# Kernel tuning notes

Measured on AMD Instinct MI355X. Metric: run time of the kernel, lower is better.

Reference implementation:

```python
import jax, jax.numpy as jnp
import numpy as np

N_EMBD = 1024
N_HEAD = 16
HEAD_DIM = N_EMBD // N_HEAD
B, T = 2, 2048
EPS = 1e-5


def setup_inputs() -> dict:
    key = jax.random.key(0)
    ks = jax.random.split(key, 12)
    s = lambda fan_in: 1.0 / np.sqrt(fan_in)
    return {
        "x": jax.random.normal(ks[0], (B, T, N_EMBD), dtype=jnp.float32),
        "ln1_g": jnp.ones((N_EMBD,), jnp.float32),
        "ln1_b": jnp.zeros((N_EMBD,), jnp.float32),
        "W_attn": jax.random.normal(ks[1], (N_EMBD, 3 * N_EMBD), jnp.float32) * s(N_EMBD),
        "b_attn": jnp.zeros((3 * N_EMBD,), jnp.float32),
        "W_proj": jax.random.normal(ks[2], (N_EMBD, N_EMBD), jnp.float32) * s(N_EMBD),
        "b_proj": jnp.zeros((N_EMBD,), jnp.float32),
        "ln2_g": jnp.ones((N_EMBD,), jnp.float32),
        "ln2_b": jnp.zeros((N_EMBD,), jnp.float32),
        "W_fc": jax.random.normal(ks[3], (N_EMBD, 4 * N_EMBD), jnp.float32) * s(N_EMBD),
        "b_fc": jnp.zeros((4 * N_EMBD,), jnp.float32),
        "W_fc2": jax.random.normal(ks[4], (4 * N_EMBD, N_EMBD), jnp.float32) * s(4 * N_EMBD),
        "b_fc2": jnp.zeros((N_EMBD,), jnp.float32),
    }


def _layernorm(x, g, b):
    mu = jnp.mean(x, axis=-1, keepdims=True)
    var = jnp.mean(jnp.square(x - mu), axis=-1, keepdims=True)
    return (x - mu) * jax.lax.rsqrt(var + EPS) * g + b


def _attention(x, W_attn, b_attn, W_proj, b_proj):
    Bsz, Tlen, C = x.shape
    qkv = x @ W_attn + b_attn  # [B,T,3C]
    q, k, v = jnp.split(qkv, 3, axis=-1)
    # [B,H,T,D]
    q = q.reshape(Bsz, Tlen, N_HEAD, HEAD_DIM).transpose(0, 2, 1, 3)
    k = k.reshape(Bsz, Tlen, N_HEAD, HEAD_DIM).transpose(0, 2, 1, 3)
    v = v.reshape(Bsz, Tlen, N_HEAD, HEAD_DIM).transpose(0, 2, 1, 3)
    att = jnp.einsum("bhqd,bhkd->bhqk", q, k) * (HEAD_DIM ** -0.5)
    causal = jnp.tril(jnp.ones((Tlen, Tlen), dtype=bool))
    att = jnp.where(causal[None, None], att, -jnp.inf)
    att = jax.nn.softmax(att, axis=-1)
    y = jnp.einsum("bhqk,bhkd->bhqd", att, v)
    y = y.transpose(0, 2, 1, 3).reshape(Bsz, Tlen, C)
    return y @ W_proj + b_proj


def _mlp(x, W_fc, b_fc, W_fc2, b_fc2):
    h = jax.nn.gelu(x @ W_fc + b_fc, approximate=False)
    return h @ W_fc2 + b_fc2


def reference(x, ln1_g, ln1_b, W_attn, b_attn, W_proj, b_proj,
              ln2_g, ln2_b, W_fc, b_fc, W_fc2, b_fc2):
    x = x + _attention(_layernorm(x, ln1_g, ln1_b), W_attn, b_attn, W_proj, b_proj)
    x = x + _mlp(_layernorm(x, ln2_g, ln2_b), W_fc, b_fc, W_fc2, b_fc2)
    return x
```

## Files before the change

### kernel.cpp

```cpp
#include <hip/hip_runtime.h>
#include <math.h>

typedef unsigned short ushort_t;
typedef __attribute__((ext_vector_type(8))) short f16x8;
typedef __attribute__((ext_vector_type(4))) float f32x4;

#define N_EMBD 1024
#define N_HEAD 16
#define HEAD_DIM 64
#define SEQ_B 2
#define SEQ_T 2048
#define M_TOK (SEQ_B * SEQ_T)

__device__ __forceinline__ ushort_t f2b(float f) {
    union { float f; unsigned int u; } v; v.f = f;
    unsigned int r = (v.u + 0x7FFFu + ((v.u >> 16) & 1u)) >> 16;
    return (ushort_t)r;
}

__device__ __forceinline__ float gelu_fast(float v) {
    float u = v + 0.044715f * v * v * v;
    float e = __expf(-1.5957691216057308f * u);
    return v * __frcp_rn(1.0f + e);
}

__device__ __forceinline__ void gload_lds16(const ushort_t* g, ushort_t* l) {
    __builtin_amdgcn_global_load_lds(
        (const __attribute__((address_space(1))) void*)g,
        (__attribute__((address_space(3))) void*)l, 16, 0, 0);
}

__global__ __launch_bounds__(256) void prep_w(
    const float* __restrict__ Wa, const float* __restrict__ Wp,
    const float* __restrict__ Wf, const float* __restrict__ Wf2,
    ushort_t* __restrict__ Ta, ushort_t* __restrict__ Tp,
    ushort_t* __restrict__ Tf, ushort_t* __restrict__ Tf2,
    const float* __restrict__ x, const float* __restrict__ g1,
    const float* __restrict__ b1, ushort_t* __restrict__ xn) {
    int b = blockIdx.x;
    int t = threadIdx.x;
    if (b >= 12288) {
        int row = b - 12288;
        const float4 v = ((const float4*)(x + (size_t)row * N_EMBD))[t];
        float s = v.x + v.y + v.z + v.w;
        float s2 = v.x * v.x + v.y * v.y + v.z * v.z + v.w * v.w;
        for (int m = 1; m < 64; m <<= 1) {
            s += __shfl_xor(s, m, 64);
            s2 += __shfl_xor(s2, m, 64);
        }
        __shared__ float ss[4], ss2[4];
        if ((t & 63) == 0) { ss[t >> 6] = s; ss2[t >> 6] = s2; }
        __syncthreads();
        s = ss[0] + ss[1] + ss[2] + ss[3];
        s2 = ss2[0] + ss2[1] + ss2[2] + ss2[3];
        float mu = s * (1.0f / N_EMBD);
        float var = s2 * (1.0f / N_EMBD) - mu * mu;
        float rs = rsqrtf(var + 1e-5f);
        const float4 gg = ((const float4*)g1)[t];
        const float4 bb = ((const float4*)b1)[t];
        ushort_t o4[4];
        o4[0] = f2b((v.x - mu) * rs * gg.x + bb.x);
        o4[1] = f2b((v.y - mu) * rs * gg.y + bb.y);
        o4[2] = f2b((v.z - mu) * rs * gg.z + bb.z);
        o4[3] = f2b((v.w - mu) * rs * gg.w + bb.w);
        *(ushort4*)(xn + (size_t)row * N_EMBD + t * 4) = *(ushort4*)o4;
        return;
    }
    __shared__ float tile[32][33];
    const float* W; ushort_t* T; int K, N, nx;
    if (b < 3072)      { W = Wa;  T = Ta;  K = 1024; N = 3072; nx = 96; }
    else if (b < 4096) { W = Wp;  T = Tp;  K = 1024; N = 1024; nx = 32; b -= 3072; }
    else if (b < 8192) { W = Wf;  T = Tf;  K = 1024; N = 4096; nx = 128; b -= 4096; }
    else               { W = Wf2; T = Tf2; K = 4096; N = 1024; nx = 32; b -= 8192; }
    int n0 = (b % nx) * 32, k0 = (b / nx) * 32;
    for (int i = 0; i < 4; ++i) {
        int l = t + i * 256; int r = l >> 5, c2 = l & 31;
        tile[r][c2] = W[(size_t)(k0 + r) * N + n0 + c2];
    }
    __syncthreads();
    for (int i = 0; i < 4; ++i) {
        int l = t + i * 256; int r = l >> 5, c2 = l & 31;
        T[(size_t)(n0 + r) * K + k0 + c2] = f2b(tile[c2][r]);
    }
}

__global__ __launch_bounds__(256) void ln2_kernel(
    const float* __restrict__ x, const float* __restrict__ g,
    const float* __restrict__ b, ushort_t* __restrict__ out) {
    int row = blockIdx.x;
    int t = threadIdx.x;
    const float4 v = ((const float4*)(x + (size_t)row * N_EMBD))[t];
    float s = v.x + v.y + v.z + v.w;
    float s2 = v.x * v.x + v.y * v.y + v.z * v.z + v.w * v.w;
    for (int m = 1; m < 64; m <<= 1) {
        s += __shfl_xor(s, m, 64);
        s2 += __shfl_xor(s2, m, 64);
    }
    __shared__ float ss[4], ss2[4];
    if ((t & 63) == 0) { ss[t >> 6] = s; ss2[t >> 6] = s2; }
    __syncthreads();
    s = ss[0] + ss[1] + ss[2] + ss[3];
    s2 = ss2[0] + ss2[1] + ss2[2] + ss2[3];
    float mu = s * (1.0f / N_EMBD);
    float var = s2 * (1.0f / N_EMBD) - mu * mu;
    float rs = rsqrtf(var + 1e-5f);
    const float4 gg = ((const float4*)g)[t];
    const float4 bb = ((const float4*)b)[t];
    ushort_t o4[4];
    o4[0] = f2b((v.x - mu) * rs * gg.x + bb.x);
    o4[1] = f2b((v.y - mu) * rs * gg.y + bb.y);
    o4[2] = f2b((v.z - mu) * rs * gg.z + bb.z);
    o4[3] = f2b((v.w - mu) * rs * gg.w + bb.w);
    *(ushort4*)(out + (size_t)row * N_EMBD + t * 4) = *(ushort4*)o4;
}

template <int MODE, int NJ>
__device__ __forceinline__ void gemm_epilogue(
    f32x4 (&acc)[4][NJ], const float* __restrict__ bias,
    const float* __restrict__ resid, void* __restrict__ Cout,
    int m0, int n0, int wr, int wc, int quad, int l16, int N) {
    for (int i = 0; i < 4; ++i) {
        for (int j = 0; j < NJ; ++j) {
            int col = n0 + wc + j * 16 + l16;
            float bv = bias[col];
            for (int r = 0; r < 4; ++r) {
                int row = m0 + wr + i * 16 + quad * 4 + r;
                float v = acc[i][j][r] + bv;
                if (MODE == 2) v = gelu_fast(v);
                if (MODE == 1 || MODE == 3) v += resid[(size_t)row * N + col];
                if (MODE == 0 || MODE == 2)
                    ((ushort_t*)Cout)[(size_t)row * N + col] = f2b(v);
                else
                    ((float*)Cout)[(size_t)row * N + col] = v;
            }
        }
    }
}

template <int MODE>
__device__ __forceinline__ void gemm_body_dma(
    const ushort_t* __restrict__ A, const ushort_t* __restrict__ Bt,
    const float* __restrict__ bias, const float* __restrict__ resid,
    void* __restrict__ Cout, int M, int N, int K) {
    __shared__ ushort_t As[2][128 * 32];
    __shared__ ushort_t Bs[2][128 * 32];
    int t = threadIdx.x;
    int wave = t >> 6, lane = t & 63;
    int quad = lane >> 4, l16 = lane & 15;
    const int swl = (l16 ^ (l16 >> 2)) & 3;
    int wr = (wave >> 1) * 64, wc = (wave & 1) * 64;
    const int m0 = blockIdx.y * 128, n0 = blockIdx.x * 128;

    const int c = wave * 64 + lane;
    const int srow = c >> 2, s_l = c & 3;
    const int s_g = s_l ^ ((srow ^ (srow >> 2)) & 3);
    const ushort_t* Ap = &A[(size_t)(m0 + srow) * K + s_g * 8];
    const ushort_t* Bp = &Bt[(size_t)(n0 + srow) * K + s_g * 8];

    const int NK = K >> 5;
    gload_lds16(Ap, &As[0][wave * 512]);
    gload_lds16(Ap + (size_t)64 * K, &As[0][wave * 512 + 2048]);
    gload_lds16(Bp, &Bs[0][wave * 512]);
    gload_lds16(Bp + (size_t)64 * K, &Bs[0][wave * 512 + 2048]);

    f32x4 acc[4][4] = {};
    for (int kt = 0; kt < NK; ++kt) {
        const int cur = kt & 1;
        __syncthreads();
        if (kt + 1 < NK) {
            const int nxt = cur ^ 1;
            const int k0 = (kt + 1) << 5;
            gload_lds16(Ap + k0, &As[nxt][wave * 512]);
            gload_lds16(Ap + (size_t)64 * K + k0, &As[nxt][wave * 512 + 2048]);
            gload_lds16(Bp + k0, &Bs[nxt][wave * 512]);
            gload_lds16(Bp + (size_t)64 * K + k0, &Bs[nxt][wave * 512 + 2048]);
        }
        f16x8 af[4], bf[4];
        for (int i = 0; i < 4; ++i)
            af[i] = *(const f16x8*)&As[cur][(wr + i * 16 + l16) * 32 + (quad ^ swl) * 8];
        for (int j = 0; j < 4; ++j)
            bf[j] = *(const f16x8*)&Bs[cur][(wc + j * 16 + l16) * 32 + (quad ^ swl) * 8];
        for (int i = 0; i < 4; ++i)
            for (int j = 0; j < 4; ++j)
                acc[i][j] = __builtin_amdgcn_mfma_f32_16x16x32_bf16(
                    af[i], bf[j], acc[i][j], 0, 0, 0);
    }
    gemm_epilogue<MODE, 4>(acc, bias, resid, Cout, m0, n0, wr, wc, quad, l16, N);
}

template <int MODE>
__device__ __forceinline__ void gemm_body_dma64(
    const ushort_t* __restrict__ A, const ushort_t* __restrict__ Bt,
    const float* __restrict__ bias, const float* __restrict__ resid,
    void* __restrict__ Cout, int M, int N, int K) {
    __shared__ ushort_t As[2][128 * 32];
    __shared__ ushort_t Bs[2][64 * 32];
    int t = threadIdx.x;
    int wave = t >> 6, lane = t & 63;
    int quad = lane >> 4, l16 = lane & 15;
    const int swl = (l16 ^ (l16 >> 2)) & 3;
    int wr = (wave >> 1) * 64, wc = (wave & 1) * 32;
    const int m0 = blockIdx.y * 128, n0 = blockIdx.x * 64;

    const int c = wave * 64 + lane;
    const int srow = c >> 2, s_l = c & 3;
    const int s_g = s_l ^ ((srow ^ (srow >> 2)) & 3);
    const ushort_t* Ap = &A[(size_t)(m0 + srow) * K + s_g * 8];
    const ushort_t* Bp = &Bt[(size_t)(n0 + srow) * K + s_g * 8];

    const int NK = K >> 5;
    gload_lds16(Ap, &As[0][wave * 512]);
    gload_lds16(Ap + (size_t)64 * K, &As[0][wave * 512 + 2048]);
    gload_lds16(Bp, &Bs[0][wave * 512]);

    f32x4 acc[4][2] = {};
    for (int kt = 0; kt < NK; ++kt) {
        const int cur = kt & 1;
        __syncthreads();
        if (kt + 1 < NK) {
            const int nxt = cur ^ 1;
            const int k0 = (kt + 1) << 5;
            gload_lds16(Ap + k0, &As[nxt][wave * 512]);
            gload_lds16(Ap + (size_t)64 * K + k0, &As[nxt][wave * 512 + 2048]);
            gload_lds16(Bp + k0, &Bs[nxt][wave * 512]);
        }
        f16x8 af[4], bf[2];
        for (int i = 0; i < 4; ++i)
            af[i] = *(const f16x8*)&As[cur][(wr + i * 16 + l16) * 32 + (quad ^ swl) * 8];
        for (int j = 0; j < 2; ++j)
            bf[j] = *(const f16x8*)&Bs[cur][(wc + j * 16 + l16) * 32 + (quad ^ swl) * 8];
        for (int i = 0; i < 4; ++i)
            for (int j = 0; j < 2; ++j)
                acc[i][j] = __builtin_amdgcn_mfma_f32_16x16x32_bf16(
                    af[i], bf[j], acc[i][j], 0, 0, 0);
    }
    gemm_epilogue<MODE, 2>(acc, bias, resid, Cout, m0, n0, wr, wc, quad, l16, N);
}

__global__ __launch_bounds__(256) void gemm_qkv(
    const ushort_t* A, const ushort_t* Bt, const float* bias, void* C,
    int M, int N, int K) { gemm_body_dma<0>(A, Bt, bias, nullptr, C, M, N, K); }
__global__ __launch_bounds__(256) void gemm_mlp1(
    const ushort_t* A, const ushort_t* Bt, const float* bias, void* C,
    int M, int N, int K) { gemm_body_dma<2>(A, Bt, bias, nullptr, C, M, N, K); }
__global__ __launch_bounds__(256) void gemm_proj(
    const ushort_t* A, const ushort_t* Bt, const float* bias,
    const float* resid, void* C, int M, int N, int K) {
    gemm_body_dma64<1>(A, Bt, bias, resid, C, M, N, K); }
__global__ __launch_bounds__(256) void gemm_out(
    const ushort_t* A, const ushort_t* Bt, const float* bias,
    const float* resid, void* C, int M, int N, int K) {
    gemm_body_dma64<3>(A, Bt, bias, resid, C, M, N, K); }

__global__ __launch_bounds__(256) void attn_kernel(
    const ushort_t* __restrict__ qkv, ushort_t* __restrict__ y) {
    const int bh = blockIdx.y;
    const int b = bh >> 4, h = bh & 15;
    const int tok0 = b * SEQ_T;
    const int t = threadIdx.x, wave = t >> 6, lane = t & 63;
    const int quad = lane >> 4, l16 = lane & 15;
    const int sw8 = l16 & 7;
    const size_t ld = 3 * N_EMBD;
    const ushort_t* Qb = qkv + (size_t)tok0 * ld + h * HEAD_DIM;
    const ushort_t* Kb = Qb + N_EMBD;
    const ushort_t* Vb = Qb + 2 * N_EMBD;

    __shared__ ushort_t Ks[64 * 64];
    __shared__ ushort_t Vt[64 * 64];
    __shared__ ushort_t Pl[4][16 * 64];

    const int kc = wave * 64 + lane;
    const int kv_s = kc >> 3, ks_l = kc & 7;
    const int ks_g = ks_l ^ (kv_s & 7);
    const ushort_t* KpL = Kb + (size_t)kv_s * ld + ks_g * 8;

    f16x8 onesB;
    for (int i = 0; i < 8; ++i) onesB[i] = (short)0x3F80;

    for (int phase = 0; phase < 2; ++phase) {
        const int qt = phase == 0 ? (int)blockIdx.x : 31 - (int)blockIdx.x;
        const int q0 = qt * 64;

        const int qrow = q0 + wave * 16 + l16;
        f16x8 qf0 = *(const f16x8*)&Qb[(size_t)qrow * ld + quad * 8];
        f16x8 qf1 = *(const f16x8*)&Qb[(size_t)qrow * ld + 32 + quad * 8];

        f32x4 o[4] = {};
        f32x4 lsum = {};

        const int nkt = qt + 1;
        for (int kt = 0; kt < nkt; ++kt) {
            __syncthreads();
            const ushort_t* kp = KpL + (size_t)kt * 64 * ld;
            gload_lds16(kp, &Ks[wave * 512]);
            gload_lds16(kp + (size_t)32 * ld, &Ks[wave * 512 + 2048]);
            for (int i = 0; i < 2; ++i) {
                int l = t + i * 256;
                int kv = l >> 3, dc = (l & 7) * 8;
                uint4 raw = *(const uint4*)&Vb[(size_t)(kt * 64 + kv) * ld + dc];
                const ushort_t* pv = (const ushort_t*)&raw;
                int pos = kv ^ ((l & 7) << 3);
                for (int e = 0; e < 8; ++e)
                    Vt[(dc + e) * 64 + pos] = pv[e];
            }
            __syncthreads();
            f32x4 s[4];
            const int ksl = (quad ^ sw8) * 8;
            for (int j = 0; j < 4; ++j) {
                const int kr = j * 16 + l16;
                f16x8 kf0 = *(const f16x8*)&Ks[kr * 64 + ksl];
                f16x8 kf1 = *(const f16x8*)&Ks[kr * 64 + (ksl ^ 32)];
                f32x4 z = {};
                z = __builtin_amdgcn_mfma_f32_16x16x32_bf16(qf0, kf0, z, 0, 0, 0);
                z = __builtin_amdgcn_mfma_f32_16x16x32_bf16(qf1, kf1, z, 0, 0, 0);
                s[j] = z;
            }
            if (kt == qt) {
                const int qr = wave * 16 + quad * 4;
                for (int j = 0; j < 4; ++j) {
                    int kg = j * 16 + l16;
                    for (int r = 0; r < 4; ++r)
                        if (kg > qr + r) s[j][r] = -INFINITY;
                }
            }
            ushort_t* myP = Pl[wave];
            for (int j = 0; j < 4; ++j) {
                int kvv = j * 16 + l16;
                int slotb = ((kvv >> 3) * 8);
                int klo = kvv & 7;
                for (int r = 0; r < 4; ++r) {
                    float p = __expf(__builtin_fmaf(s[j][r], 0.125f, -20.0f));
                    int q = quad * 4 + r;
                    myP[q * 64 + (slotb ^ ((q & 7) * 8)) + klo] = f2b(p);
                }
            }
            const int psl = (quad ^ sw8) * 8;
            f16x8 pa0 = *(const f16x8*)&myP[l16 * 64 + psl];
            f16x8 pa1 = *(const f16x8*)&myP[l16 * 64 + (psl ^ 32)];
            lsum = __builtin_amdgcn_mfma_f32_16x16x32_bf16(pa0, onesB, lsum, 0, 0, 0);
            lsum = __builtin_amdgcn_mfma_f32_16x16x32_bf16(pa1, onesB, lsum, 0, 0, 0);
            for (int dj = 0; dj < 4; ++dj) {
                const int d = dj * 16 + l16;
                const int dsw = ((d >> 3) & 7) * 8;
                f16x8 vb0 = *(const f16x8*)&Vt[d * 64 + ((quad * 8) ^ dsw)];
                f16x8 vb1 = *(const f16x8*)&Vt[d * 64 + (((quad * 8) ^ dsw) ^ 32)];
                f32x4 oo = o[dj];
                oo = __builtin_amdgcn_mfma_f32_16x16x32_bf16(pa0, vb0, oo, 0, 0, 0);
                oo = __builtin_amdgcn_mfma_f32_16x16x32_bf16(pa1, vb1, oo, 0, 0, 0);
                o[dj] = oo;
            }
        }
        float rl[4];
        for (int r = 0; r < 4; ++r) rl[r] = __frcp_rn(lsum[r]);
        for (int dj = 0; dj < 4; ++dj)
            for (int r = 0; r < 4; ++r) {
                int row = tok0 + q0 + wave * 16 + quad * 4 + r;
                int col = h * HEAD_DIM + dj * 16 + l16;
                y[(size_t)row * N_EMBD + col] = f2b(o[dj][r] * rl[r]);
            }
    }
}

extern "C" void kernel_launch(void* const* d_in, const int* in_sizes, int n_in,
                              void* d_out, int out_size, void* d_ws, size_t ws_size,
                              hipStream_t stream) {
    const float* x      = (const float*)d_in[0];
    const float* ln1_g  = (const float*)d_in[1];
    const float* ln1_b  = (const float*)d_in[2];
    const float* W_attn = (const float*)d_in[3];
    const float* b_attn = (const float*)d_in[4];
    const float* W_proj = (const float*)d_in[5];
    const float* b_proj = (const float*)d_in[6];
    const float* ln2_g  = (const float*)d_in[7];
    const float* ln2_b  = (const float*)d_in[8];
    const float* W_fc   = (const float*)d_in[9];
    const float* b_fc   = (const float*)d_in[10];
    const float* W_fc2  = (const float*)d_in[11];
    const float* b_fc2  = (const float*)d_in[12];
    float* out = (float*)d_out;

    char* w = (char*)d_ws;
    size_t o = 0;
    ushort_t* xn      = (ushort_t*)(w + o); o += (size_t)M_TOK * N_EMBD * 2;
    ushort_t* qkv     = (ushort_t*)(w + o); o += (size_t)M_TOK * 3 * N_EMBD * 2;
    ushort_t* y       = (ushort_t*)(w + o); o += (size_t)M_TOK * N_EMBD * 2;
    float*    x1      = (float*)(w + o);    o += (size_t)M_TOK * N_EMBD * 4;
    ushort_t* x1n     = (ushort_t*)(w + o); o += (size_t)M_TOK * N_EMBD * 2;
    ushort_t* hbuf    = (ushort_t*)(w + o); o += (size_t)M_TOK * 4 * N_EMBD * 2;
    ushort_t* Wt_attn = (ushort_t*)(w + o); o += (size_t)N_EMBD * 3 * N_EMBD * 2;
    ushort_t* Wt_proj = (ushort_t*)(w + o); o += (size_t)N_EMBD * N_EMBD * 2;
    ushort_t* Wt_fc   = (ushort_t*)(w + o); o += (size_t)N_EMBD * 4 * N_EMBD * 2;
    ushort_t* Wt_fc2  = (ushort_t*)(w + o); o += (size_t)4 * N_EMBD * N_EMBD * 2;

    prep_w<<<12288 + M_TOK, 256, 0, stream>>>(
        W_attn, W_proj, W_fc, W_fc2, Wt_attn, Wt_proj, Wt_fc, Wt_fc2,
        x, ln1_g, ln1_b, xn);
    gemm_qkv<<<dim3(3 * N_EMBD / 128, M_TOK / 128), 256, 0, stream>>>(
        xn, Wt_attn, b_attn, qkv, M_TOK, 3 * N_EMBD, N_EMBD);
    attn_kernel<<<dim3(SEQ_T / 128, SEQ_B * N_HEAD), 256, 0, stream>>>(qkv, y);
    gemm_proj<<<dim3(N_EMBD / 64, M_TOK / 128), 256, 0, stream>>>(
        y, Wt_proj, b_proj, x, x1, M_TOK, N_EMBD, N_EMBD);
    ln2_kernel<<<M_TOK, 256, 0, stream>>>(x1, ln2_g, ln2_b, x1n);
    gemm_mlp1<<<dim3(4 * N_EMBD / 128, M_TOK / 128), 256, 0, stream>>>(
        x1n, Wt_fc, b_fc, hbuf, M_TOK, 4 * N_EMBD, N_EMBD);
    gemm_out<<<dim3(N_EMBD / 64, M_TOK / 128), 256, 0, stream>>>(
        hbuf, Wt_fc2, b_fc2, x1, out, M_TOK, N_EMBD, 4 * N_EMBD);
    (void)in_sizes; (void)n_in; (void)out_size; (void)ws_size;
}
```

Baseline: 373.0 us.

## Split K across two wave groups inside proj and fc2 GEMM blocks

The proj and fc2 GEMMs now launch 512 threads per block. Each group of 4 waves processes half of the K dimension with its own double-buffered LDS tiles, and the partial sums are combined through LDS before the epilogue. The goal is more waves per tile and a shorter per-wave K loop, which adds latency hiding for these narrow-N GEMMs. In exchange the block uses twice the LDS and pays an extra reduction and sync, which may lower the number of blocks resident per CU.

```diff
diff --git a/kernel.cpp b/kernel.cpp
--- a/kernel.cpp
+++ b/kernel.cpp
@@ -189,29 +189,31 @@
 }
 
 template <int MODE>
-__device__ __forceinline__ void gemm_body_dma64(
+__device__ __forceinline__ void gemm_body_splitk(
     const ushort_t* __restrict__ A, const ushort_t* __restrict__ Bt,
     const float* __restrict__ bias, const float* __restrict__ resid,
     void* __restrict__ Cout, int M, int N, int K) {
-    __shared__ ushort_t As[2][128 * 32];
-    __shared__ ushort_t Bs[2][64 * 32];
+    __shared__ ushort_t As[2][2][128 * 32];
+    __shared__ ushort_t Bs[2][2][64 * 32];
     int t = threadIdx.x;
     int wave = t >> 6, lane = t & 63;
+    int half = wave >> 2, w4 = wave & 3;
     int quad = lane >> 4, l16 = lane & 15;
     const int swl = (l16 ^ (l16 >> 2)) & 3;
-    int wr = (wave >> 1) * 64, wc = (wave & 1) * 32;
+    int wr = (w4 >> 1) * 64, wc = (w4 & 1) * 32;
     const int m0 = blockIdx.y * 128, n0 = blockIdx.x * 64;
 
-    const int c = wave * 64 + lane;
+    const int K2 = K >> 1;
+    const int c = w4 * 64 + lane;
     const int srow = c >> 2, s_l = c & 3;
     const int s_g = s_l ^ ((srow ^ (srow >> 2)) & 3);
-    const ushort_t* Ap = &A[(size_t)(m0 + srow) * K + s_g * 8];
-    const ushort_t* Bp = &Bt[(size_t)(n0 + srow) * K + s_g * 8];
-
-    const int NK = K >> 5;
-    gload_lds16(Ap, &As[0][wave * 512]);
-    gload_lds16(Ap + (size_t)64 * K, &As[0][wave * 512 + 2048]);
-    gload_lds16(Bp, &Bs[0][wave * 512]);
+    const ushort_t* Ap = &A[(size_t)(m0 + srow) * K + (size_t)half * K2 + s_g * 8];
+    const ushort_t* Bp = &Bt[(size_t)(n0 + srow) * K + (size_t)half * K2 + s_g * 8];
+
+    const int NK = K2 >> 5;
+    gload_lds16(Ap, &As[0][half][w4 * 512]);
+    gload_lds16(Ap + (size_t)64 * K, &As[0][half][w4 * 512 + 2048]);
+    gload_lds16(Bp, &Bs[0][half][w4 * 512]);
 
     f32x4 acc[4][2] = {};
     for (int kt = 0; kt < NK; ++kt) {
@@ -220,21 +222,38 @@
         if (kt + 1 < NK) {
             const int nxt = cur ^ 1;
             const int k0 = (kt + 1) << 5;
-            gload_lds16(Ap + k0, &As[nxt][wave * 512]);
-            gload_lds16(Ap + (size_t)64 * K + k0, &As[nxt][wave * 512 + 2048]);
-            gload_lds16(Bp + k0, &Bs[nxt][wave * 512]);
+            gload_lds16(Ap + k0, &As[nxt][half][w4 * 512]);
+            gload_lds16(Ap + (size_t)64 * K + k0, &As[nxt][half][w4 * 512 + 2048]);
+            gload_lds16(Bp + k0, &Bs[nxt][half][w4 * 512]);
         }
         f16x8 af[4], bf[2];
         for (int i = 0; i < 4; ++i)
-            af[i] = *(const f16x8*)&As[cur][(wr + i * 16 + l16) * 32 + (quad ^ swl) * 8];
+            af[i] = *(const f16x8*)&As[cur][half][(wr + i * 16 + l16) * 32 + (quad ^ swl) * 8];
         for (int j = 0; j < 2; ++j)
-            bf[j] = *(const f16x8*)&Bs[cur][(wc + j * 16 + l16) * 32 + (quad ^ swl) * 8];
+            bf[j] = *(const f16x8*)&Bs[cur][half][(wc + j * 16 + l16) * 32 + (quad ^ swl) * 8];
         for (int i = 0; i < 4; ++i)
             for (int j = 0; j < 2; ++j)
                 acc[i][j] = __builtin_amdgcn_mfma_f32_16x16x32_bf16(
                     af[i], bf[j], acc[i][j], 0, 0, 0);
     }
-    gemm_epilogue<MODE, 2>(acc, bias, resid, Cout, m0, n0, wr, wc, quad, l16, N);
+    __syncthreads();
+    float* red = (float*)&As[0][0][0];
+    if (half == 1) {
+        for (int i = 0; i < 4; ++i)
+            for (int j = 0; j < 2; ++j)
+                for (int r = 0; r < 4; ++r)
+                    red[(wr + i * 16 + quad * 4 + r) * 64 + wc + j * 16 + l16] =
+                        acc[i][j][r];
+    }
+    __syncthreads();
+    if (half == 0) {
+        for (int i = 0; i < 4; ++i)
+            for (int j = 0; j < 2; ++j)
+                for (int r = 0; r < 4; ++r)
+                    acc[i][j][r] +=
+                        red[(wr + i * 16 + quad * 4 + r) * 64 + wc + j * 16 + l16];
+        gemm_epilogue<MODE, 2>(acc, bias, resid, Cout, m0, n0, wr, wc, quad, l16, N);
+    }
 }
 
 __global__ __launch_bounds__(256) void gemm_qkv(
@@ -243,14 +262,14 @@
 __global__ __launch_bounds__(256) void gemm_mlp1(
     const ushort_t* A, const ushort_t* Bt, const float* bias, void* C,
     int M, int N, int K) { gemm_body_dma<2>(A, Bt, bias, nullptr, C, M, N, K); }
-__global__ __launch_bounds__(256) void gemm_proj(
+__global__ __launch_bounds__(512) void gemm_proj(
     const ushort_t* A, const ushort_t* Bt, const float* bias,
     const float* resid, void* C, int M, int N, int K) {
-    gemm_body_dma64<1>(A, Bt, bias, resid, C, M, N, K); }
-__global__ __launch_bounds__(256) void gemm_out(
+    gemm_body_splitk<1>(A, Bt, bias, resid, C, M, N, K); }
+__global__ __launch_bounds__(512) void gemm_out(
     const ushort_t* A, const ushort_t* Bt, const float* bias,
     const float* resid, void* C, int M, int N, int K) {
-    gemm_body_dma64<3>(A, Bt, bias, resid, C, M, N, K); }
+    gemm_body_splitk<3>(A, Bt, bias, resid, C, M, N, K); }
 
 __global__ __launch_bounds__(256) void attn_kernel(
     const ushort_t* __restrict__ qkv, ushort_t* __restrict__ y) {
@@ -398,12 +417,12 @@
     gemm_qkv<<<dim3(3 * N_EMBD / 128, M_TOK / 128), 256, 0, stream>>>(
         xn, Wt_attn, b_attn, qkv, M_TOK, 3 * N_EMBD, N_EMBD);
     attn_kernel<<<dim3(SEQ_T / 128, SEQ_B * N_HEAD), 256, 0, stream>>>(qkv, y);
-    gemm_proj<<<dim3(N_EMBD / 64, M_TOK / 128), 256, 0, stream>>>(
+    gemm_proj<<<dim3(N_EMBD / 64, M_TOK / 128), 512, 0, stream>>>(
         y, Wt_proj, b_proj, x, x1, M_TOK, N_EMBD, N_EMBD);
     ln2_kernel<<<M_TOK, 256, 0, stream>>>(x1, ln2_g, ln2_b, x1n);
     gemm_mlp1<<<dim3(4 * N_EMBD / 128, M_TOK / 128), 256, 0, stream>>>(
         x1n, Wt_fc, b_fc, hbuf, M_TOK, 4 * N_EMBD, N_EMBD);
-    gemm_out<<<dim3(N_EMBD / 64, M_TOK / 128), 256, 0, stream>>>(
+    gemm_out<<<dim3(N_EMBD / 64, M_TOK / 128), 512, 0, stream>>>(
         hbuf, Wt_fc2, b_fc2, x1, out, M_TOK, N_EMBD, 4 * N_EMBD);
     (void)in_sizes; (void)n_in; (void)out_size; (void)ws_size;
 }
```

Result: faster. 362.5 us (-2.8%).

## Split-K proj and fc2 GEMMs with atomic accumulation; double-buffer attention K/V tiles

Applied to the files above, without the earlier changes.

The projection and second MLP GEMMs now split the K dimension across a z grid axis (2 and 4 ways) and accumulate into a buffer preinitialized with residual plus bias using float atomics. That buffer is initialized in prep_w and ln2_kernel. This raises parallelism for the N=1024 GEMMs. Separately, the attention kernel double-buffers its K and V tiles, prefetching the next tile during compute and removing one barrier per iteration. The costs are atomic traffic, nondeterministic summation order, and extra initialization writes.

```diff
diff --git a/kernel.cpp b/kernel.cpp
--- a/kernel.cpp
+++ b/kernel.cpp
@@ -36,9 +36,18 @@
     ushort_t* __restrict__ Ta, ushort_t* __restrict__ Tp,
     ushort_t* __restrict__ Tf, ushort_t* __restrict__ Tf2,
     const float* __restrict__ x, const float* __restrict__ g1,
-    const float* __restrict__ b1, ushort_t* __restrict__ xn) {
+    const float* __restrict__ b1, ushort_t* __restrict__ xn,
+    const float* __restrict__ bp, float* __restrict__ x1) {
     int b = blockIdx.x;
     int t = threadIdx.x;
+    if (b >= 12288 + M_TOK) {
+        int row = b - (12288 + M_TOK);
+        float4 v = ((const float4*)(x + (size_t)row * N_EMBD))[t];
+        const float4 bb = ((const float4*)bp)[t];
+        v.x += bb.x; v.y += bb.y; v.z += bb.z; v.w += bb.w;
+        ((float4*)(x1 + (size_t)row * N_EMBD))[t] = v;
+        return;
+    }
     if (b >= 12288) {
         int row = b - 12288;
         const float4 v = ((const float4*)(x + (size_t)row * N_EMBD))[t];
@@ -86,10 +95,18 @@
 
 __global__ __launch_bounds__(256) void ln2_kernel(
     const float* __restrict__ x, const float* __restrict__ g,
-    const float* __restrict__ b, ushort_t* __restrict__ out) {
+    const float* __restrict__ b, ushort_t* __restrict__ out,
+    const float* __restrict__ b2, float* __restrict__ outw) {
     int row = blockIdx.x;
     int t = threadIdx.x;
     const float4 v = ((const float4*)(x + (size_t)row * N_EMBD))[t];
+    {
+        const float4 bb = ((const float4*)b2)[t];
+        float4 ov;
+        ov.x = v.x + bb.x; ov.y = v.y + bb.y;
+        ov.z = v.z + bb.z; ov.w = v.w + bb.w;
+        ((float4*)(outw + (size_t)row * N_EMBD))[t] = ov;
+    }
     float s = v.x + v.y + v.z + v.w;
     float s2 = v.x * v.x + v.y * v.y + v.z * v.z + v.w * v.w;
     for (int m = 1; m < 64; m <<= 1) {
@@ -117,21 +134,22 @@
 template <int MODE, int NJ>
 __device__ __forceinline__ void gemm_epilogue(
     f32x4 (&acc)[4][NJ], const float* __restrict__ bias,
-    const float* __restrict__ resid, void* __restrict__ Cout,
+    void* __restrict__ Cout,
     int m0, int n0, int wr, int wc, int quad, int l16, int N) {
     for (int i = 0; i < 4; ++i) {
         for (int j = 0; j < NJ; ++j) {
             int col = n0 + wc + j * 16 + l16;
-            float bv = bias[col];
+            float bv = (MODE == 4) ? 0.0f : bias[col];
             for (int r = 0; r < 4; ++r) {
                 int row = m0 + wr + i * 16 + quad * 4 + r;
-                float v = acc[i][j][r] + bv;
-                if (MODE == 2) v = gelu_fast(v);
-                if (MODE == 1 || MODE == 3) v += resid[(size_t)row * N + col];
-                if (MODE == 0 || MODE == 2)
+                if (MODE == 4) {
+                    unsafeAtomicAdd(&((float*)Cout)[(size_t)row * N + col],
+                                    acc[i][j][r]);
+                } else {
+                    float v = acc[i][j][r] + bv;
+                    if (MODE == 2) v = gelu_fast(v);
                     ((ushort_t*)Cout)[(size_t)row * N + col] = f2b(v);
-                else
-                    ((float*)Cout)[(size_t)row * N + col] = v;
+                }
             }
         }
     }
@@ -140,8 +158,8 @@
 template <int MODE>
 __device__ __forceinline__ void gemm_body_dma(
     const ushort_t* __restrict__ A, const ushort_t* __restrict__ Bt,
-    const float* __restrict__ bias, const float* __restrict__ resid,
-    void* __restrict__ Cout, int M, int N, int K) {
+    const float* __restrict__ bias, void* __restrict__ Cout,
+    int M, int N, int K, int koff, int kchunk) {
     __shared__ ushort_t As[2][128 * 32];
     __shared__ ushort_t Bs[2][128 * 32];
     int t = threadIdx.x;
@@ -154,10 +172,10 @@
     const int c = wave * 64 + lane;
     const int srow = c >> 2, s_l = c & 3;
     const int s_g = s_l ^ ((srow ^ (srow >> 2)) & 3);
-    const ushort_t* Ap = &A[(size_t)(m0 + srow) * K + s_g * 8];
-    const ushort_t* Bp = &Bt[(size_t)(n0 + srow) * K + s_g * 8];
-
-    const int NK = K >> 5;
+    const ushort_t* Ap = &A[(size_t)(m0 + srow) * K + koff + s_g * 8];
+    const ushort_t* Bp = &Bt[(size_t)(n0 + srow) * K + koff + s_g * 8];
+
+    const int NK = kchunk >> 5;
     gload_lds16(Ap, &As[0][wave * 512]);
     gload_lds16(Ap + (size_t)64 * K, &As[0][wave * 512 + 2048]);
     gload_lds16(Bp, &Bs[0][wave * 512]);
@@ -185,14 +203,14 @@
                 acc[i][j] = __builtin_amdgcn_mfma_f32_16x16x32_bf16(
                     af[i], bf[j], acc[i][j], 0, 0, 0);
     }
-    gemm_epilogue<MODE, 4>(acc, bias, resid, Cout, m0, n0, wr, wc, quad, l16, N);
+    gemm_epilogue<MODE, 4>(acc, bias, Cout, m0, n0, wr, wc, quad, l16, N);
 }
 
 template <int MODE>
 __device__ __forceinline__ void gemm_body_dma64(
     const ushort_t* __restrict__ A, const ushort_t* __restrict__ Bt,
-    const float* __restrict__ bias, const float* __restrict__ resid,
-    void* __restrict__ Cout, int M, int N, int K) {
+    const float* __restrict__ bias, void* __restrict__ Cout,
+    int M, int N, int K, int koff, int kchunk) {
     __shared__ ushort_t As[2][128 * 32];
     __shared__ ushort_t Bs[2][64 * 32];
     int t = threadIdx.x;
@@ -205,10 +223,10 @@
     const int c = wave * 64 + lane;
     const int srow = c >> 2, s_l = c & 3;
     const int s_g = s_l ^ ((srow ^ (srow >> 2)) & 3);
-    const ushort_t* Ap = &A[(size_t)(m0 + srow) * K + s_g * 8];
-    const ushort_t* Bp = &Bt[(size_t)(n0 + srow) * K + s_g * 8];
-
-    const int NK = K >> 5;
+    const ushort_t* Ap = &A[(size_t)(m0 + srow) * K + koff + s_g * 8];
+    const ushort_t* Bp = &Bt[(size_t)(n0 + srow) * K + koff + s_g * 8];
+
+    const int NK = kchunk >> 5;
     gload_lds16(Ap, &As[0][wave * 512]);
     gload_lds16(Ap + (size_t)64 * K, &As[0][wave * 512 + 2048]);
     gload_lds16(Bp, &Bs[0][wave * 512]);
@@ -234,23 +252,25 @@
                 acc[i][j] = __builtin_amdgcn_mfma_f32_16x16x32_bf16(
                     af[i], bf[j], acc[i][j], 0, 0, 0);
     }
-    gemm_epilogue<MODE, 2>(acc, bias, resid, Cout, m0, n0, wr, wc, quad, l16, N);
+    gemm_epilogue<MODE, 2>(acc, bias, Cout, m0, n0, wr, wc, quad, l16, N);
 }
 
 __global__ __launch_bounds__(256) void gemm_qkv(
     const ushort_t* A, const ushort_t* Bt, const float* bias, void* C,
-    int M, int N, int K) { gemm_body_dma<0>(A, Bt, bias, nullptr, C, M, N, K); }
+    int M, int N, int K) { gemm_body_dma<0>(A, Bt, bias, C, M, N, K, 0, K); }
 __global__ __launch_bounds__(256) void gemm_mlp1(
     const ushort_t* A, const ushort_t* Bt, const float* bias, void* C,
-    int M, int N, int K) { gemm_body_dma<2>(A, Bt, bias, nullptr, C, M, N, K); }
+    int M, int N, int K) { gemm_body_dma<2>(A, Bt, bias, C, M, N, K, 0, K); }
 __global__ __launch_bounds__(256) void gemm_proj(
-    const ushort_t* A, const ushort_t* Bt, const float* bias,
-    const float* resid, void* C, int M, int N, int K) {
-    gemm_body_dma64<1>(A, Bt, bias, resid, C, M, N, K); }
+    const ushort_t* A, const ushort_t* Bt, void* C, int M, int N, int K) {
+    const int kc = K >> 1;
+    gemm_body_dma64<4>(A, Bt, nullptr, C, M, N, K, blockIdx.z * kc, kc);
+}
 __global__ __launch_bounds__(256) void gemm_out(
-    const ushort_t* A, const ushort_t* Bt, const float* bias,
-    const float* resid, void* C, int M, int N, int K) {
-    gemm_body_dma64<3>(A, Bt, bias, resid, C, M, N, K); }
+    const ushort_t* A, const ushort_t* Bt, void* C, int M, int N, int K) {
+    const int kc = K >> 2;
+    gemm_body_dma<4>(A, Bt, nullptr, C, M, N, K, blockIdx.z * kc, kc);
+}
 
 __global__ __launch_bounds__(256) void attn_kernel(
     const ushort_t* __restrict__ qkv, ushort_t* __restrict__ y) {
@@ -265,8 +285,8 @@
     const ushort_t* Kb = Qb + N_EMBD;
     const ushort_t* Vb = Qb + 2 * N_EMBD;
 
-    __shared__ ushort_t Ks[64 * 64];
-    __shared__ ushort_t Vt[64 * 64];
+    __shared__ ushort_t Ks[2][64 * 64];
+    __shared__ ushort_t Vt[2][64 * 64];
     __shared__ ushort_t Pl[4][16 * 64];
 
     const int kc = wave * 64 + lane;
@@ -274,6 +294,11 @@
     const int ks_g = ks_l ^ (kv_s & 7);
     const ushort_t* KpL = Kb + (size_t)kv_s * ld + ks_g * 8;
 
+    const int v_kv0 = t >> 3, v_dc0 = (t & 7) * 8;
+    const int v_pos0 = v_kv0 ^ ((t & 7) << 3);
+    const int v_kv1 = (t + 256) >> 3, v_dc1 = v_dc0;
+    const int v_pos1 = v_kv1 ^ ((t & 7) << 3);
+
     f16x8 onesB;
     for (int i = 0; i < 8; ++i) onesB[i] = (short)0x3F80;
 
@@ -289,27 +314,37 @@
         f32x4 lsum = {};
 
         const int nkt = qt + 1;
+
+        __syncthreads();
+        gload_lds16(KpL, &Ks[0][wave * 512]);
+        gload_lds16(KpL + (size_t)32 * ld, &Ks[0][wave * 512 + 2048]);
+        {
+            uint4 r0 = *(const uint4*)&Vb[(size_t)v_kv0 * ld + v_dc0];
+            uint4 r1 = *(const uint4*)&Vb[(size_t)v_kv1 * ld + v_dc1];
+            const ushort_t* p0 = (const ushort_t*)&r0;
+            const ushort_t* p1 = (const ushort_t*)&r1;
+            for (int e = 0; e < 8; ++e) Vt[0][(v_dc0 + e) * 64 + v_pos0] = p0[e];
+            for (int e = 0; e < 8; ++e) Vt[0][(v_dc1 + e) * 64 + v_pos1] = p1[e];
+        }
+
         for (int kt = 0; kt < nkt; ++kt) {
+            const int cur = kt & 1;
             __syncthreads();
-            const ushort_t* kp = KpL + (size_t)kt * 64 * ld;
-            gload_lds16(kp, &Ks[wave * 512]);
-            gload_lds16(kp + (size_t)32 * ld, &Ks[wave * 512 + 2048]);
-            for (int i = 0; i < 2; ++i) {
-                int l = t + i * 256;
-                int kv = l >> 3, dc = (l & 7) * 8;
-                uint4 raw = *(const uint4*)&Vb[(size_t)(kt * 64 + kv) * ld + dc];
-                const ushort_t* pv = (const ushort_t*)&raw;
-                int pos = kv ^ ((l & 7) << 3);
-                for (int e = 0; e < 8; ++e)
-                    Vt[(dc + e) * 64 + pos] = pv[e];
-            }
-            __syncthreads();
+            const bool pf = (kt + 1 < nkt);
+            uint4 vr0, vr1;
+            if (pf) {
+                vr0 = *(const uint4*)&Vb[(size_t)((kt + 1) * 64 + v_kv0) * ld + v_dc0];
+                vr1 = *(const uint4*)&Vb[(size_t)((kt + 1) * 64 + v_kv1) * ld + v_dc1];
+                const ushort_t* kp = KpL + (size_t)(kt + 1) * 64 * ld;
+                gload_lds16(kp, &Ks[cur ^ 1][wave * 512]);
+                gload_lds16(kp + (size_t)32 * ld, &Ks[cur ^ 1][wave * 512 + 2048]);
+            }
             f32x4 s[4];
             const int ksl = (quad ^ sw8) * 8;
             for (int j = 0; j < 4; ++j) {
                 const int kr = j * 16 + l16;
-                f16x8 kf0 = *(const f16x8*)&Ks[kr * 64 + ksl];
-                f16x8 kf1 = *(const f16x8*)&Ks[kr * 64 + (ksl ^ 32)];
+                f16x8 kf0 = *(const f16x8*)&Ks[cur][kr * 64 + ksl];
+                f16x8 kf1 = *(const f16x8*)&Ks[cur][kr * 64 + (ksl ^ 32)];
                 f32x4 z = {};
                 z = __builtin_amdgcn_mfma_f32_16x16x32_bf16(qf0, kf0, z, 0, 0, 0);
                 z = __builtin_amdgcn_mfma_f32_16x16x32_bf16(qf1, kf1, z, 0, 0, 0);
@@ -342,12 +377,19 @@
             for (int dj = 0; dj < 4; ++dj) {
                 const int d = dj * 16 + l16;
                 const int dsw = ((d >> 3) & 7) * 8;
-                f16x8 vb0 = *(const f16x8*)&Vt[d * 64 + ((quad * 8) ^ dsw)];
-                f16x8 vb1 = *(const f16x8*)&Vt[d * 64 + (((quad * 8) ^ dsw) ^ 32)];
+                f16x8 vb0 = *(const f16x8*)&Vt[cur][d * 64 + ((quad * 8) ^ dsw)];
+                f16x8 vb1 = *(const f16x8*)&Vt[cur][d * 64 + (((quad * 8) ^ dsw) ^ 32)];
                 f32x4 oo = o[dj];
                 oo = __builtin_amdgcn_mfma_f32_16x16x32_bf16(pa0, vb0, oo, 0, 0, 0);
                 oo = __builtin_amdgcn_mfma_f32_16x16x32_bf16(pa1, vb1, oo, 0, 0, 0);
                 o[dj] = oo;
+            }
+            if (pf) {
+                const ushort_t* p0 = (const ushort_t*)&vr0;
+                const ushort_t* p1 = (const ushort_t*)&vr1;
+                ushort_t* Vn = Vt[cur ^ 1];
+                for (int e = 0; e < 8; ++e) Vn[(v_dc0 + e) * 64 + v_pos0] = p0[e];
+                for (int e = 0; e < 8; ++e) Vn[(v_dc1 + e) * 64 + v_pos1] = p1[e];
             }
         }
         float rl[4];
@@ -392,18 +434,18 @@
     ushort_t* Wt_fc   = (ushort_t*)(w + o); o += (size_t)N_EMBD * 4 * N_EMBD * 2;
     ushort_t* Wt_fc2  = (ushort_t*)(w + o); o += (size_t)4 * N_EMBD * N_EMBD * 2;
 
-    prep_w<<<12288 + M_TOK, 256, 0, stream>>>(
+    prep_w<<<12288 + 2 * M_TOK, 256, 0, stream>>>(
         W_attn, W_proj, W_fc, W_fc2, Wt_attn, Wt_proj, Wt_fc, Wt_fc2,
-        x, ln1_g, ln1_b, xn);
+        x, ln1_g, ln1_b, xn, b_proj, x1);
     gemm_qkv<<<dim3(3 * N_EMBD / 128, M_TOK / 128), 256, 0, stream>>>(
         xn, Wt_attn, b_attn, qkv, M_TOK, 3 * N_EMBD, N_EMBD);
     attn_kernel<<<dim3(SEQ_T / 128, SEQ_B * N_HEAD), 256, 0, stream>>>(qkv, y);
-    gemm_proj<<<dim3(N_EMBD / 64, M_TOK / 128), 256, 0, stream>>>(
-        y, Wt_proj, b_proj, x, x1, M_TOK, N_EMBD, N_EMBD);
-    ln2_kernel<<<M_TOK, 256, 0, stream>>>(x1, ln2_g, ln2_b, x1n);
+    gemm_proj<<<dim3(N_EMBD / 64, M_TOK / 128, 2), 256, 0, stream>>>(
+        y, Wt_proj, x1, M_TOK, N_EMBD, N_EMBD);
+    ln2_kernel<<<M_TOK, 256, 0, stream>>>(x1, ln2_g, ln2_b, x1n, b_fc2, out);
     gemm_mlp1<<<dim3(4 * N_EMBD / 128, M_TOK / 128), 256, 0, stream>>>(
         x1n, Wt_fc, b_fc, hbuf, M_TOK, 4 * N_EMBD, N_EMBD);
-    gemm_out<<<dim3(N_EMBD / 64, M_TOK / 128), 256, 0, stream>>>(
-        hbuf, Wt_fc2, b_fc2, x1, out, M_TOK, N_EMBD, 4 * N_EMBD);
+    gemm_out<<<dim3(N_EMBD / 128, M_TOK / 128, 4), 256, 0, stream>>>(
+        hbuf, Wt_fc2, out, M_TOK, N_EMBD, 4 * N_EMBD);
     (void)in_sizes; (void)n_in; (void)out_size; (void)ws_size;
 }
```

Measured after the change: 406.6 us. +9.0%, slower.
